# Kernel optimization log

Measured on AMD Instinct MI355X. Metric: run time of the kernel, lower is better.

The kernel has to match this reference:

```python
import jax, jax.numpy as jnp
import numpy as np

ALPHA = 1.0
BETA = 0.05


def setup_inputs() -> dict:
    key = jax.random.key(0)
    kQ, kK, kV, kH, kDQ, kDK = jax.random.split(key, 6)
    N, M, D, d = 8192, 8192, 128, 128
    Q = jax.random.normal(kQ, (N, D), dtype=jnp.float32)
    K = jax.random.normal(kK, (M, D), dtype=jnp.float32)
    V = jax.random.normal(kV, (M, d), dtype=jnp.float32)
    # Doob h-potential must be strictly positive (it is logged)
    h = jax.random.uniform(kH, (N,), dtype=jnp.float32, minval=0.5, maxval=1.5)
    log_d_q = 0.1 * jax.random.normal(kDQ, (N,), dtype=jnp.float32)
    log_d_k = 0.1 * jax.random.normal(kDK, (M,), dtype=jnp.float32)
    return {"Q": Q, "K": K, "V": V, "h": h, "log_d_q": log_d_q, "log_d_k": log_d_k}


def reference(Q, K, V, h, log_d_q, log_d_k):
    # s_ij = -beta*||q_i - k_j||^2 - alpha*(log_d_q[i] + log_d_k[j]) + log h_i - log h_j
    q_norm2 = jnp.sum(Q * Q, axis=-1)  # (N,)
    k_norm2 = jnp.sum(K * K, axis=-1)  # (M,)
    log_h = jnp.log(h)                  # (N,) ; Q and K share h (self-attention points)
    qk = jnp.einsum("nd,md->nm", Q, K)  # (N, M)
    s = BETA * (2.0 * qk - q_norm2[:, None] - k_norm2[None, :])
    s = s - ALPHA * (log_d_q[:, None] + log_d_k[None, :])
    s = s + log_h[:, None] - log_h[None, :]
    # row-softmax = Markov normalisation; lse = log row sums of un-normalised kernel
    lse = jax.nn.logsumexp(s, axis=-1)          # (N,)
    P = jnp.exp(s - lse[:, None])               # (N, M)
    out = jnp.einsum("nm,md->nd", P, V)          # (N, d)
    return out, lse
```

## Files before the change

### kernel.cpp

```cpp
#include <hip/hip_runtime.h>
#include <cstddef>
#include <cstdint>

#define BETA 0.05f

typedef unsigned short u16;
typedef unsigned int u32;
typedef __attribute__((ext_vector_type(8))) short bf16x8;
typedef __attribute__((ext_vector_type(16))) float f32x16;
typedef __attribute__((ext_vector_type(4))) u32 u32x4;

constexpr int NQ = 8192;
constexpr int NK = 8192;
constexpr int DH = 128;
constexpr int DA = 144;
constexpr int SPLITS = 8;
constexpr int CHUNK = NK / SPLITS;
constexpr int KVB = 32;
constexpr int STEPS = CHUNK / KVB;
constexpr int KSTRIDE = 304;
constexpr int KTILE = 32 * KSTRIDE;
constexpr int VSTRIDE = 80;
constexpr int VTILE = 128 * VSTRIDE;

__device__ __forceinline__ u16 f2bf(float x) {
  union { float f; u32 u; } v; v.f = x;
  u32 r = (v.u + 0x7fffu + ((v.u >> 16) & 1u)) >> 16;
  return (u16)r;
}
__device__ __forceinline__ float fexp2(float x) {
#if __has_builtin(__builtin_amdgcn_exp2f)
  return __builtin_amdgcn_exp2f(x);
#else
  return exp2f(x);
#endif
}

__global__ void prep_q(const float* __restrict__ Q, const float* __restrict__ ldq,
                       const float* __restrict__ h, u16* __restrict__ Qa,
                       float* __restrict__ arow) {
  const int row = blockIdx.x * 4 + (threadIdx.x >> 6);
  const int lane = threadIdx.x & 63;
  const float2 q2 = *(const float2*)(Q + (size_t)row * DH + lane * 2);
  float sq = q2.x * q2.x + q2.y * q2.y;
#pragma unroll
  for (int off = 32; off > 0; off >>= 1) sq += __shfl_xor(sq, off);
  const float SC = 2.0f * BETA * 1.4426950408889634f;
  ushort2 o; o.x = f2bf(SC * q2.x); o.y = f2bf(SC * q2.y);
  *(ushort2*)(Qa + (size_t)row * DA + lane * 2) = o;
  if (lane < 8) {
    ushort2 a;
    if (lane == 0) { a.x = 0x3F80; a.y = 0x3F80; } else { a.x = 0; a.y = 0; }
    *(ushort2*)(Qa + (size_t)row * DA + 128 + lane * 2) = a;
  }
  if (lane == 0) arow[row] = -BETA * sq - ldq[row] + logf(h[row]);
}

__global__ void prep_k(const float* __restrict__ K, const float* __restrict__ ldk,
                       const float* __restrict__ h, u16* __restrict__ Ka) {
  const int row = blockIdx.x * 4 + (threadIdx.x >> 6);
  const int lane = threadIdx.x & 63;
  const float2 k2 = *(const float2*)(K + (size_t)row * DH + lane * 2);
  float sq = k2.x * k2.x + k2.y * k2.y;
#pragma unroll
  for (int off = 32; off > 0; off >>= 1) sq += __shfl_xor(sq, off);
  ushort2 o; o.x = f2bf(k2.x); o.y = f2bf(k2.y);
  *(ushort2*)(Ka + (size_t)row * DA + lane * 2) = o;
  if (lane < 8) {
    ushort2 a; a.x = 0; a.y = 0;
    if (lane == 0) {
      const float b2 = (-BETA * sq - ldk[row] - logf(h[row])) * 1.4426950408889634f;
      const u16 bh = f2bf(b2);
      union { u32 u; float f; } hf; hf.u = ((u32)bh) << 16;
      const u16 bl = f2bf(b2 - hf.f);
      a.x = bh; a.y = bl;
    }
    *(ushort2*)(Ka + (size_t)row * DA + 128 + lane * 2) = a;
  }
}

__global__ void prep_vt(const float* __restrict__ V, u16* __restrict__ VTb) {
  __shared__ float tile[64][65];
  const int j0 = blockIdx.x * 64;
  const int d0 = blockIdx.y * 64;
  const int t = threadIdx.x;
  const int r = t >> 4;
  const int c = (t & 15) * 4;
#pragma unroll
  for (int rr = r; rr < 64; rr += 16) {
    const float4 v = *(const float4*)(V + (size_t)(j0 + rr) * DH + d0 + c);
    tile[rr][c + 0] = v.x; tile[rr][c + 1] = v.y;
    tile[rr][c + 2] = v.z; tile[rr][c + 3] = v.w;
  }
  __syncthreads();
#pragma unroll
  for (int dd = r; dd < 64; dd += 16) {
    ushort4 o;
    o.x = f2bf(tile[c + 0][dd]);
    o.y = f2bf(tile[c + 1][dd]);
    o.z = f2bf(tile[c + 2][dd]);
    o.w = f2bf(tile[c + 3][dd]);
    *(ushort4*)(VTb + (size_t)(d0 + dd) * NK + j0 + c) = o;
  }
}

__global__ __launch_bounds__(512, 2) void attn_main(
    const u16* __restrict__ Qa, const u16* __restrict__ Ka,
    const u16* __restrict__ VTb, float* __restrict__ Opart,
    float* __restrict__ Lpart) {
  __shared__ __align__(16) char lds[2 * KTILE + 2 * VTILE];
  char* ldsK = lds;
  char* ldsV = lds + 2 * KTILE;

  const int tid = threadIdx.x;
  const int wid = tid >> 6;
  const int lane = tid & 63;
  const int hi = lane >> 5;
  const int ln31 = lane & 31;
  const int bi = blockIdx.x;
  const int ks = bi & 7;
  const int qg = bi >> 3;
  const int kvbase = ks * CHUNK;
  const int qrow0 = qg * 256 + wid * 32;

  bf16x8 qf[9];
#pragma unroll
  for (int sl = 0; sl < 9; ++sl)
    qf[sl] = *(const bf16x8*)((const char*)Qa + (size_t)(qrow0 + ln31) * 288 + sl * 32 + hi * 16);

  f32x16 acc[4];
#pragma unroll
  for (int dt = 0; dt < 4; ++dt)
#pragma unroll
    for (int r = 0; r < 16; ++r) acc[dt][r] = 0.0f;
  float lsum = 0.0f;

  u32x4 kreg0, kreg1, vreg;
  const char* KaB = (const char*)Ka;
  const char* VTB = (const char*)VTb;

  auto issueLoads = [&](int step) {
    const char* ksrc = KaB + (size_t)(kvbase + step * KVB) * 288;
    kreg0 = *(const u32x4*)(ksrc + (tid >> 4) * 288 + (tid & 15) * 16);
    if (tid < 64)
      kreg1 = *(const u32x4*)(ksrc + (tid >> 1) * 288 + 256 + (tid & 1) * 16);
    const char* vsrc = VTB + (size_t)(tid >> 2) * (NK * 2) + (size_t)(kvbase + step * KVB) * 2;
    vreg = *(const u32x4*)(vsrc + (tid & 3) * 16);
  };
  auto writeLds = [&](int buf) {
    char* kd = ldsK + buf * KTILE;
    *(u32x4*)(kd + (tid >> 4) * KSTRIDE + (tid & 15) * 16) = kreg0;
    if (tid < 64)
      *(u32x4*)(kd + (tid >> 1) * KSTRIDE + 256 + (tid & 1) * 16) = kreg1;
    char* vd = ldsV + buf * VTILE;
    *(u32x4*)(vd + (tid >> 2) * VSTRIDE + (tid & 3) * 16) = vreg;
  };

  issueLoads(0);
  writeLds(0);
  __syncthreads();

  for (int t = 0; t < STEPS; ++t) {
    const int cur = t & 1;
    if (t < STEPS - 1) issueLoads(t + 1);

    const char* kb = ldsK + cur * KTILE;
    const char* vb = ldsV + cur * VTILE;

    f32x16 sA, sB;
#pragma unroll
    for (int r = 0; r < 16; ++r) { sA[r] = 0.0f; sB[r] = 0.0f; }
#pragma unroll
    for (int sl = 0; sl < 9; ++sl) {
      const bf16x8 kf = *(const bf16x8*)(kb + ln31 * KSTRIDE + sl * 32 + hi * 16);
      if (sl & 1)
        sB = __builtin_amdgcn_mfma_f32_32x32x16_bf16(kf, qf[sl], sB, 0, 0, 0);
      else
        sA = __builtin_amdgcn_mfma_f32_32x32x16_bf16(kf, qf[sl], sA, 0, 0, 0);
    }

    float p[16];
#pragma unroll
    for (int r = 0; r < 16; ++r) p[r] = fexp2(sA[r] + sB[r]);
    {
      float t0 = (p[0] + p[1]) + (p[2] + p[3]);
      float t1 = (p[4] + p[5]) + (p[6] + p[7]);
      float t2 = (p[8] + p[9]) + (p[10] + p[11]);
      float t3 = (p[12] + p[13]) + (p[14] + p[15]);
      lsum += (t0 + t1) + (t2 + t3);
    }

    u32 pk0, pk1, pk2, pk3, pk4, pk5, pk6, pk7;
    asm("v_cvt_pk_bf16_f32 %0, %1, %2" : "=v"(pk0) : "v"(p[0]),  "v"(p[1]));
    asm("v_cvt_pk_bf16_f32 %0, %1, %2" : "=v"(pk1) : "v"(p[2]),  "v"(p[3]));
    asm("v_cvt_pk_bf16_f32 %0, %1, %2" : "=v"(pk2) : "v"(p[4]),  "v"(p[5]));
    asm("v_cvt_pk_bf16_f32 %0, %1, %2" : "=v"(pk3) : "v"(p[6]),  "v"(p[7]));
    asm("v_cvt_pk_bf16_f32 %0, %1, %2" : "=v"(pk4) : "v"(p[8]),  "v"(p[9]));
    asm("v_cvt_pk_bf16_f32 %0, %1, %2" : "=v"(pk5) : "v"(p[10]), "v"(p[11]));
    asm("v_cvt_pk_bf16_f32 %0, %1, %2" : "=v"(pk6) : "v"(p[12]), "v"(p[13]));
    asm("v_cvt_pk_bf16_f32 %0, %1, %2" : "=v"(pk7) : "v"(p[14]), "v"(p[15]));
    const bool hb = (hi != 0);

#pragma unroll
    for (int ksl = 0; ksl < 2; ++ksl) {
      const u32 a0 = ksl ? pk4 : pk0, a1 = ksl ? pk5 : pk1;
      const u32 b0 = ksl ? pk6 : pk2, b1 = ksl ? pk7 : pk3;
      const u32 own0 = hb ? b0 : a0, own1 = hb ? b1 : a1;
      const u32 snd0 = hb ? a0 : b0, snd1 = hb ? a1 : b1;
      const u32 rcv0 = (u32)__shfl_xor((int)snd0, 32);
      const u32 rcv1 = (u32)__shfl_xor((int)snd1, 32);
      union { u32x4 u; bf16x8 b; } pa;
      pa.u[0] = hb ? rcv0 : own0;
      pa.u[1] = hb ? rcv1 : own1;
      pa.u[2] = hb ? own0 : rcv0;
      pa.u[3] = hb ? own1 : rcv1;
#pragma unroll
      for (int dt = 0; dt < 4; ++dt) {
        const bf16x8 vf = *(const bf16x8*)(vb + (dt * 32 + ln31) * VSTRIDE + ksl * 32 + hi * 16);
        acc[dt] = __builtin_amdgcn_mfma_f32_32x32x16_bf16(pa.b, vf, acc[dt], 0, 0, 0);
      }
    }

    if (t < STEPS - 1) {
      writeLds(cur ^ 1);
      __syncthreads();
    }
  }

  lsum += __shfl_xor(lsum, 32);
  float* op = Opart + ((size_t)ks * NQ + qrow0) * DH;
#pragma unroll
  for (int dt = 0; dt < 4; ++dt)
#pragma unroll
    for (int r = 0; r < 16; ++r) {
      const int q = (r & 3) + 8 * (r >> 2) + 4 * hi;
      op[(size_t)q * DH + dt * 32 + ln31] = acc[dt][r];
    }
  if (hi == 0) Lpart[(size_t)ks * NQ + qrow0 + ln31] = lsum;
}

__global__ void combine(const float* __restrict__ Opart, const float* __restrict__ Lpart,
                        const float* __restrict__ arow, float* __restrict__ out,
                        float* __restrict__ lse) {
  const int idx = blockIdx.x * 256 + threadIdx.x;
  const int row = idx >> 5;
  const int d4 = (idx & 31) * 4;
  float4 o = make_float4(0.f, 0.f, 0.f, 0.f);
  float L = 0.f;
#pragma unroll
  for (int s = 0; s < SPLITS; ++s) {
    const float4 v = *(const float4*)(Opart + ((size_t)s * NQ + row) * DH + d4);
    o.x += v.x; o.y += v.y; o.z += v.z; o.w += v.w;
    L += Lpart[(size_t)s * NQ + row];
  }
  const float inv = 1.0f / L;
  *(float4*)(out + (size_t)row * DH + d4) =
      make_float4(o.x * inv, o.y * inv, o.z * inv, o.w * inv);
  if ((idx & 31) == 0) lse[row] = logf(L) + arow[row];
}

extern "C" void kernel_launch(void* const* d_in, const int* in_sizes, int n_in,
                              void* d_out, int out_size, void* d_ws, size_t ws_size,
                              hipStream_t stream) {
  const float* Q = (const float*)d_in[0];
  const float* K = (const float*)d_in[1];
  const float* V = (const float*)d_in[2];
  const float* h = (const float*)d_in[3];
  const float* ldq = (const float*)d_in[4];
  const float* ldk = (const float*)d_in[5];

  char* ws = (char*)d_ws;
  u16* Qa    = (u16*)(ws + 0);
  u16* Ka    = (u16*)(ws + 2359296);
  u16* VTb   = (u16*)(ws + 4718592);
  float* arow  = (float*)(ws + 6815744);
  float* Opart = (float*)(ws + 6848512);
  float* Lpart = (float*)(ws + 40402944);

  float* out = (float*)d_out;
  float* lse = out + (size_t)NQ * DH;

  prep_q<<<NQ / 4, 256, 0, stream>>>(Q, ldq, h, Qa, arow);
  prep_k<<<NK / 4, 256, 0, stream>>>(K, ldk, h, Ka);
  prep_vt<<<dim3(NK / 64, DH / 64), 256, 0, stream>>>(V, VTb);
  attn_main<<<32 * SPLITS, 512, 0, stream>>>(Qa, Ka, VTb, Opart, Lpart);
  combine<<<NQ * 32 / 256, 256, 0, stream>>>(Opart, Lpart, arow, out, lse);
}
```

Measured before the change: 66.47 us.

## Use 16 KV splits, 256-thread blocks, bf16 partials, and merged Q/K prep

```diff
diff --git a/kernel.cpp b/kernel.cpp
--- a/kernel.cpp
+++ b/kernel.cpp
@@ -14,10 +14,11 @@
 constexpr int NK = 8192;
 constexpr int DH = 128;
 constexpr int DA = 144;
-constexpr int SPLITS = 8;
+constexpr int SPLITS = 16;
 constexpr int CHUNK = NK / SPLITS;
 constexpr int KVB = 32;
 constexpr int STEPS = CHUNK / KVB;
+constexpr int WV = 4;
 constexpr int KSTRIDE = 304;
 constexpr int KTILE = 32 * KSTRIDE;
 constexpr int VSTRIDE = 80;
@@ -28,54 +29,48 @@
   u32 r = (v.u + 0x7fffu + ((v.u >> 16) & 1u)) >> 16;
   return (u16)r;
 }
-__device__ __forceinline__ float fexp2(float x) {
-#if __has_builtin(__builtin_amdgcn_exp2f)
-  return __builtin_amdgcn_exp2f(x);
-#else
-  return exp2f(x);
-#endif
-}
-
-__global__ void prep_q(const float* __restrict__ Q, const float* __restrict__ ldq,
-                       const float* __restrict__ h, u16* __restrict__ Qa,
-                       float* __restrict__ arow) {
-  const int row = blockIdx.x * 4 + (threadIdx.x >> 6);
+__device__ __forceinline__ float fexp2(float x) { return exp2f(x); }
+
+__global__ void prep_qk(const float* __restrict__ Q, const float* __restrict__ ldq,
+                        const float* __restrict__ K, const float* __restrict__ ldk,
+                        const float* __restrict__ h, u16* __restrict__ Qa,
+                        u16* __restrict__ Ka, float* __restrict__ arow) {
+  const int bi = blockIdx.x;
   const int lane = threadIdx.x & 63;
-  const float2 q2 = *(const float2*)(Q + (size_t)row * DH + lane * 2);
-  float sq = q2.x * q2.x + q2.y * q2.y;
-#pragma unroll
-  for (int off = 32; off > 0; off >>= 1) sq += __shfl_xor(sq, off);
-  const float SC = 2.0f * BETA * 1.4426950408889634f;
-  ushort2 o; o.x = f2bf(SC * q2.x); o.y = f2bf(SC * q2.y);
-  *(ushort2*)(Qa + (size_t)row * DA + lane * 2) = o;
-  if (lane < 8) {
-    ushort2 a;
-    if (lane == 0) { a.x = 0x3F80; a.y = 0x3F80; } else { a.x = 0; a.y = 0; }
-    *(ushort2*)(Qa + (size_t)row * DA + 128 + lane * 2) = a;
-  }
-  if (lane == 0) arow[row] = -BETA * sq - ldq[row] + logf(h[row]);
-}
-
-__global__ void prep_k(const float* __restrict__ K, const float* __restrict__ ldk,
-                       const float* __restrict__ h, u16* __restrict__ Ka) {
-  const int row = blockIdx.x * 4 + (threadIdx.x >> 6);
-  const int lane = threadIdx.x & 63;
-  const float2 k2 = *(const float2*)(K + (size_t)row * DH + lane * 2);
-  float sq = k2.x * k2.x + k2.y * k2.y;
-#pragma unroll
-  for (int off = 32; off > 0; off >>= 1) sq += __shfl_xor(sq, off);
-  ushort2 o; o.x = f2bf(k2.x); o.y = f2bf(k2.y);
-  *(ushort2*)(Ka + (size_t)row * DA + lane * 2) = o;
-  if (lane < 8) {
-    ushort2 a; a.x = 0; a.y = 0;
-    if (lane == 0) {
-      const float b2 = (-BETA * sq - ldk[row] - logf(h[row])) * 1.4426950408889634f;
-      const u16 bh = f2bf(b2);
-      union { u32 u; float f; } hf; hf.u = ((u32)bh) << 16;
-      const u16 bl = f2bf(b2 - hf.f);
-      a.x = bh; a.y = bl;
-    }
-    *(ushort2*)(Ka + (size_t)row * DA + 128 + lane * 2) = a;
+  if (bi < NQ / 4) {
+    const int row = bi * 4 + (threadIdx.x >> 6);
+    const float2 q2 = *(const float2*)(Q + (size_t)row * DH + lane * 2);
+    float sq = q2.x * q2.x + q2.y * q2.y;
+#pragma unroll
+    for (int off = 32; off > 0; off >>= 1) sq += __shfl_xor(sq, off);
+    const float SC = 2.0f * BETA * 1.4426950408889634f;
+    ushort2 o; o.x = f2bf(SC * q2.x); o.y = f2bf(SC * q2.y);
+    *(ushort2*)(Qa + (size_t)row * DA + lane * 2) = o;
+    if (lane < 8) {
+      ushort2 a;
+      if (lane == 0) { a.x = 0x3F80; a.y = 0x3F80; } else { a.x = 0; a.y = 0; }
+      *(ushort2*)(Qa + (size_t)row * DA + 128 + lane * 2) = a;
+    }
+    if (lane == 0) arow[row] = -BETA * sq - ldq[row] + logf(h[row]);
+  } else {
+    const int row = (bi - NQ / 4) * 4 + (threadIdx.x >> 6);
+    const float2 k2 = *(const float2*)(K + (size_t)row * DH + lane * 2);
+    float sq = k2.x * k2.x + k2.y * k2.y;
+#pragma unroll
+    for (int off = 32; off > 0; off >>= 1) sq += __shfl_xor(sq, off);
+    ushort2 o; o.x = f2bf(k2.x); o.y = f2bf(k2.y);
+    *(ushort2*)(Ka + (size_t)row * DA + lane * 2) = o;
+    if (lane < 8) {
+      ushort2 a; a.x = 0; a.y = 0;
+      if (lane == 0) {
+        const float b2 = (-BETA * sq - ldk[row] - logf(h[row])) * 1.4426950408889634f;
+        const u16 bh = f2bf(b2);
+        union { u32 u; float f; } hf; hf.u = ((u32)bh) << 16;
+        const u16 bl = f2bf(b2 - hf.f);
+        a.x = bh; a.y = bl;
+      }
+      *(ushort2*)(Ka + (size_t)row * DA + 128 + lane * 2) = a;
+    }
   }
 }
 
@@ -104,9 +99,9 @@
   }
 }
 
-__global__ __launch_bounds__(512, 2) void attn_main(
+__global__ __launch_bounds__(256, 3) void attn_main(
     const u16* __restrict__ Qa, const u16* __restrict__ Ka,
-    const u16* __restrict__ VTb, float* __restrict__ Opart,
+    const u16* __restrict__ VTb, u16* __restrict__ Opart,
     float* __restrict__ Lpart) {
   __shared__ __align__(16) char lds[2 * KTILE + 2 * VTILE];
   char* ldsK = lds;
@@ -118,10 +113,10 @@
   const int hi = lane >> 5;
   const int ln31 = lane & 31;
   const int bi = blockIdx.x;
-  const int ks = bi & 7;
-  const int qg = bi >> 3;
+  const int ks = bi & 15;
+  const int qg = bi >> 4;
   const int kvbase = ks * CHUNK;
-  const int qrow0 = qg * 256 + wid * 32;
+  const int qrow0 = qg * 128 + wid * 32;
 
   bf16x8 qf[9];
 #pragma unroll
@@ -135,25 +130,29 @@
     for (int r = 0; r < 16; ++r) acc[dt][r] = 0.0f;
   float lsum = 0.0f;
 
-  u32x4 kreg0, kreg1, vreg;
+  u32x4 kreg0, kreg1, kreg2, vreg0, vreg1;
   const char* KaB = (const char*)Ka;
   const char* VTB = (const char*)VTb;
 
   auto issueLoads = [&](int step) {
     const char* ksrc = KaB + (size_t)(kvbase + step * KVB) * 288;
     kreg0 = *(const u32x4*)(ksrc + (tid >> 4) * 288 + (tid & 15) * 16);
+    kreg1 = *(const u32x4*)(ksrc + (16 + (tid >> 4)) * 288 + (tid & 15) * 16);
     if (tid < 64)
-      kreg1 = *(const u32x4*)(ksrc + (tid >> 1) * 288 + 256 + (tid & 1) * 16);
-    const char* vsrc = VTB + (size_t)(tid >> 2) * (NK * 2) + (size_t)(kvbase + step * KVB) * 2;
-    vreg = *(const u32x4*)(vsrc + (tid & 3) * 16);
+      kreg2 = *(const u32x4*)(ksrc + (tid >> 1) * 288 + 256 + (tid & 1) * 16);
+    const char* vsrc = VTB + (size_t)(kvbase + step * KVB) * 2;
+    vreg0 = *(const u32x4*)(vsrc + (size_t)(tid >> 2) * (NK * 2) + (tid & 3) * 16);
+    vreg1 = *(const u32x4*)(vsrc + (size_t)(64 + (tid >> 2)) * (NK * 2) + (tid & 3) * 16);
   };
   auto writeLds = [&](int buf) {
     char* kd = ldsK + buf * KTILE;
     *(u32x4*)(kd + (tid >> 4) * KSTRIDE + (tid & 15) * 16) = kreg0;
+    *(u32x4*)(kd + (16 + (tid >> 4)) * KSTRIDE + (tid & 15) * 16) = kreg1;
     if (tid < 64)
-      *(u32x4*)(kd + (tid >> 1) * KSTRIDE + 256 + (tid & 1) * 16) = kreg1;
+      *(u32x4*)(kd + (tid >> 1) * KSTRIDE + 256 + (tid & 1) * 16) = kreg2;
     char* vd = ldsV + buf * VTILE;
-    *(u32x4*)(vd + (tid >> 2) * VSTRIDE + (tid & 3) * 16) = vreg;
+    *(u32x4*)(vd + (tid >> 2) * VSTRIDE + (tid & 3) * 16) = vreg0;
+    *(u32x4*)(vd + (64 + (tid >> 2)) * VSTRIDE + (tid & 3) * 16) = vreg1;
   };
 
   issueLoads(0);
@@ -228,34 +227,37 @@
   }
 
   lsum += __shfl_xor(lsum, 32);
-  float* op = Opart + ((size_t)ks * NQ + qrow0) * DH;
+  u16* op = Opart + ((size_t)ks * NQ + qrow0) * DH;
 #pragma unroll
   for (int dt = 0; dt < 4; ++dt)
 #pragma unroll
     for (int r = 0; r < 16; ++r) {
       const int q = (r & 3) + 8 * (r >> 2) + 4 * hi;
-      op[(size_t)q * DH + dt * 32 + ln31] = acc[dt][r];
+      op[(size_t)q * DH + dt * 32 + ln31] = f2bf(acc[dt][r]);
     }
   if (hi == 0) Lpart[(size_t)ks * NQ + qrow0 + ln31] = lsum;
 }
 
-__global__ void combine(const float* __restrict__ Opart, const float* __restrict__ Lpart,
+__global__ void combine(const u16* __restrict__ Opart, const float* __restrict__ Lpart,
                         const float* __restrict__ arow, float* __restrict__ out,
                         float* __restrict__ lse) {
   const int idx = blockIdx.x * 256 + threadIdx.x;
   const int row = idx >> 5;
   const int d4 = (idx & 31) * 4;
-  float4 o = make_float4(0.f, 0.f, 0.f, 0.f);
+  float o0 = 0.f, o1 = 0.f, o2 = 0.f, o3 = 0.f;
   float L = 0.f;
 #pragma unroll
   for (int s = 0; s < SPLITS; ++s) {
-    const float4 v = *(const float4*)(Opart + ((size_t)s * NQ + row) * DH + d4);
-    o.x += v.x; o.y += v.y; o.z += v.z; o.w += v.w;
+    const ushort4 v = *(const ushort4*)(Opart + ((size_t)s * NQ + row) * DH + d4);
+    union { u32 u; float f; } c0, c1, c2, c3;
+    c0.u = ((u32)v.x) << 16; c1.u = ((u32)v.y) << 16;
+    c2.u = ((u32)v.z) << 16; c3.u = ((u32)v.w) << 16;
+    o0 += c0.f; o1 += c1.f; o2 += c2.f; o3 += c3.f;
     L += Lpart[(size_t)s * NQ + row];
   }
   const float inv = 1.0f / L;
   *(float4*)(out + (size_t)row * DH + d4) =
-      make_float4(o.x * inv, o.y * inv, o.z * inv, o.w * inv);
+      make_float4(o0 * inv, o1 * inv, o2 * inv, o3 * inv);
   if ((idx & 31) == 0) lse[row] = logf(L) + arow[row];
 }
 
@@ -274,15 +276,14 @@
   u16* Ka    = (u16*)(ws + 2359296);
   u16* VTb   = (u16*)(ws + 4718592);
   float* arow  = (float*)(ws + 6815744);
-  float* Opart = (float*)(ws + 6848512);
+  u16* Opart = (u16*)(ws + 6848512);
   float* Lpart = (float*)(ws + 40402944);
 
   float* out = (float*)d_out;
   float* lse = out + (size_t)NQ * DH;
 
-  prep_q<<<NQ / 4, 256, 0, stream>>>(Q, ldq, h, Qa, arow);
-  prep_k<<<NK / 4, 256, 0, stream>>>(K, ldk, h, Ka);
+  prep_qk<<<NQ / 2, 256, 0, stream>>>(Q, ldq, K, ldk, h, Qa, Ka, arow);
   prep_vt<<<dim3(NK / 64, DH / 64), 256, 0, stream>>>(V, VTb);
-  attn_main<<<32 * SPLITS, 512, 0, stream>>>(Qa, Ka, VTb, Opart, Lpart);
+  attn_main<<<(NQ / 128) * SPLITS, 256, 0, stream>>>(Qa, Ka, VTb, Opart, Lpart);
   combine<<<NQ * 32 / 256, 256, 0, stream>>>(Opart, Lpart, arow, out, lse);
 }
```

Result: slower. 76.69 us (+15.4%).
